# Kernel tuning notes

Measured on AMD Instinct MI355X. Metric: run time of the kernel, lower is better.

## Reference

```python
import math
import jax, jax.numpy as jnp
import numpy as np

B, L, H = 32, 1024, 128

def setup_inputs() -> dict:
    key = jax.random.key(0)
    k1, k2, k3, k4 = jax.random.split(key, 4)
    a = jax.random.normal(k1, (B, L, H), dtype=jnp.float32)
    b = jax.random.normal(k2, (B, L, H), dtype=jnp.float32)
    mask_a = jax.random.randint(k3, (B, L, 1), 0, 2, dtype=jnp.int32)
    mask_b = jax.random.randint(k4, (B, L, 1), 0, 2, dtype=jnp.int32)
    temperature = jnp.asarray(1.0 / math.sqrt(H), dtype=jnp.float32)
    return {"a": a, "b": b, "mask_a": mask_a, "mask_b": mask_b, "temperature": temperature}

def reference(a, b, mask_a, mask_b, temperature):
    # scores: [B, La, Lb]
    scores = jnp.einsum('bld,bmd->blm', a, b) * temperature
    # outer product of token validity masks -> pair mask [B, La, Lb]
    mask = jnp.einsum('blk,bmk->blm', mask_a.astype(jnp.float32), mask_b.astype(jnp.float32)) > 0
    scores = jnp.where(mask, scores, jnp.float32(-10000.0))
    attention_a = jax.nn.softmax(scores, axis=1)  # normalize over La (columns)
    attention_b = jax.nn.softmax(scores, axis=2)  # normalize over Lb (rows)
    feature_a = jnp.einsum('blm,bmd->bld', attention_b, b)
    feature_b = jnp.einsum('blm,bmd->bld', attention_a, a)  # valid since La == Lb
    return (feature_a, feature_b)
```

## Files before the change

kernel.cpp:

```cpp
#include <hip/hip_runtime.h>
#include <math.h>

#define BN 32
#define LL 1024
#define HH 128

typedef __attribute__((ext_vector_type(8))) short short8;
typedef __attribute__((ext_vector_type(4))) float f32x4;

static const size_t SZ_BF = (size_t)BN * LL * HH * 2;

__device__ __forceinline__ ushort f2bf(float x) {
  union { float f; unsigned u; } c; c.f = x;
  unsigned r = c.u + 0x7fffu + ((c.u >> 16) & 1u);
  return (ushort)(r >> 16);
}
__device__ __forceinline__ float bf2f(ushort h) {
  union { unsigned u; float f; } c; c.u = ((unsigned)h) << 16;
  return c.f;
}
__device__ __forceinline__ short8 ld8(const ushort* p) {
  return *(const short8*)p;
}

__global__ __launch_bounds__(256) void k_convert(
    const float* __restrict__ a, const float* __restrict__ b,
    const int* __restrict__ mask_b,
    ushort* __restrict__ abf, ushort* __restrict__ bbf,
    ushort* __restrict__ aT, ushort* __restrict__ bT,
    float* __restrict__ meanb, float* __restrict__ invmean) {
  int bb = blockIdx.y;
  int l0 = blockIdx.x * 64;
  int which = blockIdx.z;
  const float* src = which ? b : a;
  ushort* dst  = which ? bbf : abf;
  ushort* dstT = which ? bT : aT;
  float* dmean = which ? meanb : invmean;
  __shared__ __align__(16) ushort T[128][72];
  __shared__ float accS[128];
  __shared__ float wgt[64];
  int t = threadIdx.x;
  if (t < 128) accS[t] = 0.f;
  if (t < 64)
    wgt[t] = which ? 1.0f : ((mask_b[bb * LL + l0 + t] == 0) ? 1.0f : 0.0f);
  int lrow = t >> 5;
  int dcol = (t & 31) * 4;
#pragma unroll
  for (int p = 0; p < 8; ++p) {
    int l = p * 8 + lrow;
    float4 v = *(const float4*)&src[((size_t)bb * LL + l0 + l) * HH + dcol];
    ushort4 u;
    u.x = f2bf(v.x); u.y = f2bf(v.y); u.z = f2bf(v.z); u.w = f2bf(v.w);
    *(ushort4*)&dst[((size_t)bb * LL + l0 + l) * HH + dcol] = u;
    T[dcol + 0][l] = u.x; T[dcol + 1][l] = u.y;
    T[dcol + 2][l] = u.z; T[dcol + 3][l] = u.w;
  }
  __syncthreads();
  int drow = t >> 3;
  int c8 = (t & 7) * 8;
#pragma unroll
  for (int q = 0; q < 4; ++q) {
    int d = q * 32 + drow;
    short8 val = *(const short8*)&T[d][c8];
    *(short8*)&dstT[((size_t)bb * HH + d) * LL + l0 + c8] = val;
    float s = 0.f;
#pragma unroll
    for (int j = 0; j < 8; ++j) s += wgt[c8 + j] * bf2f((ushort)val[j]);
    atomicAdd(&accS[d], s);
  }
  __syncthreads();
  if (t < 128) atomicAdd(&dmean[bb * HH + t], accS[t]);
}


__global__ __launch_bounds__(256, 2) void k_colsum(
    const ushort* __restrict__ abf, const ushort* __restrict__ bbf,
    const int* __restrict__ mask_a, const int* __restrict__ mask_b,
    const float* __restrict__ temp_p, float2* __restrict__ cc) {
  int wg = blockIdx.x;
  int xcd = wg & 7, k_ = wg >> 3;
  int bb = (k_ >> 4) * 8 + xcd;
  int m0 = (k_ & 15) * 64;
  int t = threadIdx.x;
  int w = t >> 6, lane = t & 63, l16 = lane & 15, quad = lane >> 4;
  float temp = temp_p[0];
  __shared__ __align__(16) float biasA[LL];
  __shared__ float csred[4][4][16];
  for (int i = t; i < LL; i += 256)
    biasA[i] = mask_a[bb * LL + i] ? 0.0f : -10000.0f;

  short8 Bm[4][4];
  float biasB_mt[4];
#pragma unroll
  for (int mt = 0; mt < 4; ++mt) {
    int m = m0 + mt * 16 + l16;
    biasB_mt[mt] = mask_b[bb * LL + m] ? 0.0f : -10000.0f;
#pragma unroll
    for (int k = 0; k < 4; ++k)
      Bm[mt][k] = ld8(&bbf[((size_t)bb * LL + m) * HH + k * 32 + quad * 8]);
  }
  __syncthreads();

  float cs[4] = {0.f, 0.f, 0.f, 0.f};
  short8 Al0[4], Al1[4];

#define LOADAL(AlX, IT)                                                       \
  {                                                                           \
    const ushort* arow = &abf[((size_t)bb * LL + w * 256 + (IT) * 16 + l16) * HH]; \
    _Pragma("unroll") for (int k = 0; k < 4; ++k)                             \
        AlX[k] = ld8(&arow[k * 32 + quad * 8]);                               \
  }

#define CSCOMPUTE(AlX, IT)                                                    \
  {                                                                           \
    int lbase = w * 256 + (IT) * 16;                                          \
    f32x4 bA = *(const f32x4*)&biasA[lbase + quad * 4];                       \
    _Pragma("unroll") for (int mt = 0; mt < 4; ++mt) {                        \
      f32x4 sacc = {0.f, 0.f, 0.f, 0.f};                                      \
      _Pragma("unroll") for (int k = 0; k < 4; ++k)                           \
          sacc = __builtin_amdgcn_mfma_f32_16x16x32_bf16(AlX[k], Bm[mt][k],   \
                                                         sacc, 0, 0, 0);      \
      _Pragma("unroll") for (int r = 0; r < 4; ++r)                           \
          cs[mt] += __expf(sacc[r] * temp + bA[r] + biasB_mt[mt]);            \
    }                                                                         \
  }

  LOADAL(Al0, 0);
  for (int it = 0; it < 16; it += 2) {
    LOADAL(Al1, it + 1);
    CSCOMPUTE(Al0, it);
    LOADAL(Al0, (it + 2) & 15);
    CSCOMPUTE(Al1, it + 1);
  }
#undef LOADAL
#undef CSCOMPUTE

#pragma unroll
  for (int mt = 0; mt < 4; ++mt) {
    cs[mt] += __shfl_xor(cs[mt], 16);
    cs[mt] += __shfl_xor(cs[mt], 32);
  }
  if (lane < 16) {
#pragma unroll
    for (int mt = 0; mt < 4; ++mt) csred[w][mt][l16] = cs[mt];
  }
  __syncthreads();
  if (t < 64) {
    int mt = t >> 4, ml = t & 15;
    float s = csred[0][mt][ml] + csred[1][mt][ml] + csred[2][mt][ml] + csred[3][mt][ml];
    int m = m0 + t;
    float bB = mask_b[bb * LL + m] ? 0.0f : -10000.0f;
    cc[bb * LL + m] = make_float2(s > 0.f ? 1.0f / s : 0.0f, bB);
  }
}

__global__ __launch_bounds__(256, 2) void k_features(
    const ushort* __restrict__ abf, const ushort* __restrict__ bbf,
    const ushort* __restrict__ aT, const ushort* __restrict__ bT,
    const int* __restrict__ mask_a, const float* __restrict__ temp_p,
    const float2* __restrict__ cc, const float* __restrict__ meanb,
    const float* __restrict__ invmean, float* __restrict__ out) {
  int wg = blockIdx.x;
  int xcd = wg & 7, k_ = wg >> 3;
  int bb = (k_ >> 4) * 8 + xcd;
  int l0 = (k_ & 15) * 64;
  int t = threadIdx.x;
  int w = t >> 6, lane = t & 63, l16 = lane & 15, quad = lane >> 4;
  float temp = temp_p[0];

  __shared__ float2 ccs[LL];
  __shared__ __align__(16) ushort Pa[2][64 * 72];
  __shared__ __align__(16) ushort Pb[2][64 * 72];
  __shared__ float rspart[4][64];
  __shared__ float rsfin[64];

  for (int i = t; i < LL; i += 256) ccs[i] = cc[bb * LL + i];

  float biasA_lt[4];
  short8 Afix[4][4];
#pragma unroll
  for (int lt = 0; lt < 4; ++lt) {
    int l = l0 + lt * 16 + l16;
    biasA_lt[lt] = mask_a[bb * LL + l] ? 0.0f : -10000.0f;
#pragma unroll
    for (int k = 0; k < 4; ++k)
      Afix[lt][k] = ld8(&abf[((size_t)bb * LL + l) * HH + k * 32 + quad * 8]);
  }

  f32x4 accA[4][2], accB[4][2];
  f32x4 zero = {0.f, 0.f, 0.f, 0.f};
#pragma unroll
  for (int lt = 0; lt < 4; ++lt)
#pragma unroll
    for (int dt = 0; dt < 2; ++dt) { accA[lt][dt] = zero; accB[lt][dt] = zero; }
  float rs_lt[4] = {0.f, 0.f, 0.f, 0.f};
  __syncthreads();

  short8 Am0[4], Am1[4];
  float2 cv0[4], cv1[4];
  short8 Bb0[2][2], Ba0[2][2], Bb1[2][2], Ba1[2][2];

#define LOADAM(AmX, cvX, M0)                                                  \
  {                                                                           \
    const ushort* brow = &bbf[((size_t)bb * LL + (M0) + w * 16 + l16) * HH];  \
    _Pragma("unroll") for (int k = 0; k < 4; ++k)                             \
        AmX[k] = ld8(&brow[k * 32 + quad * 8]);                               \
    _Pragma("unroll") for (int r = 0; r < 4; ++r)                             \
        cvX[r] = ccs[(M0) + w * 16 + quad * 4 + r];                           \
  }

#define LOADBT(BbX, BaX, M0)                                                  \
  {                                                                           \
    _Pragma("unroll") for (int dt = 0; dt < 2; ++dt) {                        \
      const ushort* btrow =                                                   \
          &bT[((size_t)bb * HH + w * 32 + dt * 16 + l16) * LL + (M0)];        \
      const ushort* atrow =                                                   \
          &aT[((size_t)bb * HH + w * 32 + dt * 16 + l16) * LL + (M0)];        \
      _Pragma("unroll") for (int ks = 0; ks < 2; ++ks) {                      \
        BbX[dt][ks] = ld8(&btrow[ks * 32 + quad * 8]);                        \
        BaX[dt][ks] = ld8(&atrow[ks * 32 + quad * 8]);                        \
      }                                                                       \
    }                                                                         \
  }

#define SPHASE(AmX, cvX, PBUFI)                                               \
  {                                                                           \
    ushort* pa = &Pa[PBUFI][0];                                               \
    ushort* pb = &Pb[PBUFI][0];                                               \
    _Pragma("unroll") for (int lt = 0; lt < 4; ++lt) {                        \
      f32x4 sacc = zero;                                                      \
      _Pragma("unroll") for (int k = 0; k < 4; ++k)                           \
          sacc = __builtin_amdgcn_mfma_f32_16x16x32_bf16(AmX[k], Afix[lt][k], \
                                                         sacc, 0, 0, 0);      \
      ushort pav[4], pbv[4];                                                  \
      _Pragma("unroll") for (int r = 0; r < 4; ++r) {                         \
        float e = __expf(sacc[r] * temp + biasA_lt[lt] + cvX[r].y);           \
        pav[r] = f2bf(e);                                                     \
        rs_lt[lt] += bf2f(pav[r]);                                            \
        pbv[r] = f2bf(e * cvX[r].x);                                          \
      }                                                                       \
      uint2 ka, kb;                                                           \
      ka.x = (uint)pav[0] | ((uint)pav[1] << 16);                             \
      ka.y = (uint)pav[2] | ((uint)pav[3] << 16);                             \
      kb.x = (uint)pbv[0] | ((uint)pbv[1] << 16);                             \
      kb.y = (uint)pbv[2] | ((uint)pbv[3] << 16);                             \
      int pidx = (lt * 16 + l16) * 72 + w * 16 + quad * 4;                    \
      *(uint2*)&pa[pidx] = ka;                                                \
      *(uint2*)&pb[pidx] = kb;                                                \
    }                                                                         \
  }

#define FPHASE(PBUFI, BbX, BaX)                                               \
  {                                                                           \
    const ushort* pa = &Pa[PBUFI][0];                                         \
    const ushort* pb = &Pb[PBUFI][0];                                         \
    _Pragma("unroll") for (int lt = 0; lt < 4; ++lt) {                        \
      _Pragma("unroll") for (int ks = 0; ks < 2; ++ks) {                      \
        int ridx = (lt * 16 + l16) * 72 + ks * 32 + quad * 8;                 \
        short8 PaF = *(const short8*)&pa[ridx];                               \
        short8 PbF = *(const short8*)&pb[ridx];                               \
        _Pragma("unroll") for (int dt = 0; dt < 2; ++dt) {                    \
          accA[lt][dt] = __builtin_amdgcn_mfma_f32_16x16x32_bf16(             \
              PaF, BbX[dt][ks], accA[lt][dt], 0, 0, 0);                       \
          accB[lt][dt] = __builtin_amdgcn_mfma_f32_16x16x32_bf16(             \
              PbF, BaX[dt][ks], accB[lt][dt], 0, 0, 0);                       \
        }                                                                     \
      }                                                                       \
    }                                                                         \
  }

  LOADAM(Am0, cv0, 0);
  LOADBT(Bb0, Ba0, 0);
  LOADAM(Am1, cv1, 64);
  SPHASE(Am0, cv0, 0);
  __syncthreads();

  for (int kk = 0; kk < 7; ++kk) {
    int mA = (2 * kk + 1) * 64;
    LOADBT(Bb1, Ba1, mA);
    LOADAM(Am0, cv0, mA + 64);
    SPHASE(Am1, cv1, 1);
    FPHASE(0, Bb0, Ba0);
    __syncthreads();
    LOADBT(Bb0, Ba0, mA + 64);
    LOADAM(Am1, cv1, mA + 128);
    SPHASE(Am0, cv0, 0);
    FPHASE(1, Bb1, Ba1);
    __syncthreads();
  }

  LOADBT(Bb1, Ba1, 960);
  SPHASE(Am1, cv1, 1);
  FPHASE(0, Bb0, Ba0);
  __syncthreads();
  FPHASE(1, Bb1, Ba1);

#undef LOADAM
#undef LOADBT
#undef SPHASE
#undef FPHASE

#pragma unroll
  for (int lt = 0; lt < 4; ++lt) {
    rs_lt[lt] += __shfl_xor(rs_lt[lt], 16);
    rs_lt[lt] += __shfl_xor(rs_lt[lt], 32);
  }
  if (lane < 16) {
#pragma unroll
    for (int lt = 0; lt < 4; ++lt) rspart[w][lt * 16 + l16] = rs_lt[lt];
  }
  __syncthreads();
  if (t < 64)
    rsfin[t] = rspart[0][t] + rspart[1][t] + rspart[2][t] + rspart[3][t];
  __syncthreads();

  float* outA = out;
  float* outB = out + (size_t)BN * LL * HH;
#pragma unroll
  for (int dt = 0; dt < 2; ++dt) {
    int d = w * 32 + dt * 16 + l16;
    float mb = meanb[bb * HH + d] * (1.0f / 1024.0f);
    float im = invmean[bb * HH + d] * (1.0f / 1024.0f);
#pragma unroll
    for (int lt = 0; lt < 4; ++lt) {
#pragma unroll
      for (int r = 0; r < 4; ++r) {
        int l = lt * 16 + quad * 4 + r;
        float rsv = rsfin[l];
        float fa = (rsv > 0.f) ? accA[lt][dt][r] / rsv : mb;
        float fb = accB[lt][dt][r] + im;
        __builtin_nontemporal_store(fa, &outA[((size_t)bb * LL + l0 + l) * HH + d]);
        __builtin_nontemporal_store(fb, &outB[((size_t)bb * LL + l0 + l) * HH + d]);
      }
    }
  }
}

extern "C" void kernel_launch(void* const* d_in, const int* in_sizes, int n_in,
                              void* d_out, int out_size, void* d_ws, size_t ws_size,
                              hipStream_t stream) {
  const float* a = (const float*)d_in[0];
  const float* b = (const float*)d_in[1];
  const int* mask_a = (const int*)d_in[2];
  const int* mask_b = (const int*)d_in[3];
  const float* temp = (const float*)d_in[4];
  float* out = (float*)d_out;

  char* wsb = (char*)d_ws;
  ushort* abf = (ushort*)(wsb + 0 * SZ_BF);
  ushort* bbf = (ushort*)(wsb + 1 * SZ_BF);
  ushort* aT  = (ushort*)(wsb + 2 * SZ_BF);
  ushort* bT  = (ushort*)(wsb + 3 * SZ_BF);
  float2* cc  = (float2*)(wsb + 4 * SZ_BF);
  float* meanb   = (float*)(wsb + 4 * SZ_BF + (size_t)BN * LL * sizeof(float2));
  float* invmean = meanb + BN * HH;

  hipMemsetAsync(meanb, 0, 2 * BN * HH * sizeof(float), stream);
  k_convert<<<dim3(16, 32, 2), 256, 0, stream>>>(a, b, mask_b, abf, bbf, aT, bT,
                                                 meanb, invmean);
  k_colsum<<<dim3(512), 256, 0, stream>>>(abf, bbf, mask_a, mask_b, temp, cc);
  k_features<<<dim3(512), 256, 0, stream>>>(abf, bbf, aT, bT, mask_a, temp,
                                            cc, meanb, invmean, out);
  (void)in_sizes; (void)n_in; (void)out_size; (void)ws_size;
}
```

Measured before the change: 200.7 us.

## Fold column-softmax normalization into transposed A instead of a second P tile

The column-sum kernel now scales the transposed bf16 copy of A in place by each column's inverse softmax sum. The feature kernel can then reuse the single unnormalized P tile for both MFMA products. This drops the second LDS P buffer, its bf16 conversions, and its LDS writes and reads in the inner loop. In exchange, the colsum kernel does an extra read-modify-write pass over aT, and rounding shifts because the scaling is applied to A rather than to P.

```diff
diff --git a/kernel.cpp b/kernel.cpp
--- a/kernel.cpp
+++ b/kernel.cpp
@@ -75,6 +75,7 @@
 
 __global__ __launch_bounds__(256, 2) void k_colsum(
     const ushort* __restrict__ abf, const ushort* __restrict__ bbf,
+    ushort* __restrict__ aTm,
     const int* __restrict__ mask_a, const int* __restrict__ mask_b,
     const float* __restrict__ temp_p, float2* __restrict__ cc) {
   int wg = blockIdx.x;
@@ -86,6 +87,7 @@
   float temp = temp_p[0];
   __shared__ __align__(16) float biasA[LL];
   __shared__ float csred[4][4][16];
+  __shared__ float invS[64];
   for (int i = t; i < LL; i += 256)
     biasA[i] = mask_a[bb * LL + i] ? 0.0f : -10000.0f;
 
@@ -150,7 +152,28 @@
     float s = csred[0][mt][ml] + csred[1][mt][ml] + csred[2][mt][ml] + csred[3][mt][ml];
     int m = m0 + t;
     float bB = mask_b[bb * LL + m] ? 0.0f : -10000.0f;
-    cc[bb * LL + m] = make_float2(s > 0.f ? 1.0f / s : 0.0f, bB);
+    float inv = s > 0.f ? 1.0f / s : 0.0f;
+    invS[t] = inv;
+    cc[bb * LL + m] = make_float2(inv, bB);
+  }
+  __syncthreads();
+
+  {
+    int d = t >> 1, mc = (t & 1) * 32;
+    ushort* ap = &aTm[((size_t)bb * HH + d) * LL + m0 + mc];
+    short8 v0 = ld8(ap), v1 = ld8(ap + 8), v2 = ld8(ap + 16), v3 = ld8(ap + 24);
+    ushort o[32];
+#pragma unroll
+    for (int j = 0; j < 8; ++j) {
+      o[j]      = f2bf(bf2f((ushort)v0[j]) * invS[mc + j]);
+      o[8 + j]  = f2bf(bf2f((ushort)v1[j]) * invS[mc + 8 + j]);
+      o[16 + j] = f2bf(bf2f((ushort)v2[j]) * invS[mc + 16 + j]);
+      o[24 + j] = f2bf(bf2f((ushort)v3[j]) * invS[mc + 24 + j]);
+    }
+    *(short8*)ap        = *(short8*)&o[0];
+    *(short8*)(ap + 8)  = *(short8*)&o[8];
+    *(short8*)(ap + 16) = *(short8*)&o[16];
+    *(short8*)(ap + 24) = *(short8*)&o[24];
   }
 }
 
@@ -170,7 +193,6 @@
 
   __shared__ float2 ccs[LL];
   __shared__ __align__(16) ushort Pa[2][64 * 72];
-  __shared__ __align__(16) ushort Pb[2][64 * 72];
   __shared__ float rspart[4][64];
   __shared__ float rsfin[64];
 
@@ -197,7 +219,7 @@
   __syncthreads();
 
   short8 Am0[4], Am1[4];
-  float2 cv0[4], cv1[4];
+  float cv0[4], cv1[4];
   short8 Bb0[2][2], Ba0[2][2], Bb1[2][2], Ba1[2][2];
 
 #define LOADAM(AmX, cvX, M0)                                                  \
@@ -206,7 +228,7 @@
     _Pragma("unroll") for (int k = 0; k < 4; ++k)                             \
         AmX[k] = ld8(&brow[k * 32 + quad * 8]);                               \
     _Pragma("unroll") for (int r = 0; r < 4; ++r)                             \
-        cvX[r] = ccs[(M0) + w * 16 + quad * 4 + r];                           \
+        cvX[r] = ccs[(M0) + w * 16 + quad * 4 + r].y;                         \
   }
 
 #define LOADBT(BbX, BaX, M0)                                                  \
@@ -226,44 +248,37 @@
 #define SPHASE(AmX, cvX, PBUFI)                                               \
   {                                                                           \
     ushort* pa = &Pa[PBUFI][0];                                               \
-    ushort* pb = &Pb[PBUFI][0];                                               \
     _Pragma("unroll") for (int lt = 0; lt < 4; ++lt) {                        \
       f32x4 sacc = zero;                                                      \
       _Pragma("unroll") for (int k = 0; k < 4; ++k)                           \
           sacc = __builtin_amdgcn_mfma_f32_16x16x32_bf16(AmX[k], Afix[lt][k], \
                                                          sacc, 0, 0, 0);      \
-      ushort pav[4], pbv[4];                                                  \
+      ushort pav[4];                                                          \
       _Pragma("unroll") for (int r = 0; r < 4; ++r) {                         \
-        float e = __expf(sacc[r] * temp + biasA_lt[lt] + cvX[r].y);           \
+        float e = __expf(sacc[r] * temp + biasA_lt[lt] + cvX[r]);             \
         pav[r] = f2bf(e);                                                     \
         rs_lt[lt] += bf2f(pav[r]);                                            \
-        pbv[r] = f2bf(e * cvX[r].x);                                          \
       }                                                                       \
-      uint2 ka, kb;                                                           \
+      uint2 ka;                                                               \
       ka.x = (uint)pav[0] | ((uint)pav[1] << 16);                             \
       ka.y = (uint)pav[2] | ((uint)pav[3] << 16);                             \
-      kb.x = (uint)pbv[0] | ((uint)pbv[1] << 16);                             \
-      kb.y = (uint)pbv[2] | ((uint)pbv[3] << 16);                             \
       int pidx = (lt * 16 + l16) * 72 + w * 16 + quad * 4;                    \
       *(uint2*)&pa[pidx] = ka;                                                \
-      *(uint2*)&pb[pidx] = kb;                                                \
     }                                                                         \
   }
 
 #define FPHASE(PBUFI, BbX, BaX)                                               \
   {                                                                           \
     const ushort* pa = &Pa[PBUFI][0];                                         \
-    const ushort* pb = &Pb[PBUFI][0];                                         \
     _Pragma("unroll") for (int lt = 0; lt < 4; ++lt) {                        \
       _Pragma("unroll") for (int ks = 0; ks < 2; ++ks) {                      \
         int ridx = (lt * 16 + l16) * 72 + ks * 32 + quad * 8;                 \
         short8 PaF = *(const short8*)&pa[ridx];                               \
-        short8 PbF = *(const short8*)&pb[ridx];                               \
         _Pragma("unroll") for (int dt = 0; dt < 2; ++dt) {                    \
           accA[lt][dt] = __builtin_amdgcn_mfma_f32_16x16x32_bf16(             \
               PaF, BbX[dt][ks], accA[lt][dt], 0, 0, 0);                       \
           accB[lt][dt] = __builtin_amdgcn_mfma_f32_16x16x32_bf16(             \
-              PbF, BaX[dt][ks], accB[lt][dt], 0, 0, 0);                       \
+              PaF, BaX[dt][ks], accB[lt][dt], 0, 0, 0);                       \
         }                                                                     \
       }                                                                       \
     }                                                                         \
@@ -358,7 +373,7 @@
   hipMemsetAsync(meanb, 0, 2 * BN * HH * sizeof(float), stream);
   k_convert<<<dim3(16, 32, 2), 256, 0, stream>>>(a, b, mask_b, abf, bbf, aT, bT,
                                                  meanb, invmean);
-  k_colsum<<<dim3(512), 256, 0, stream>>>(abf, bbf, mask_a, mask_b, temp, cc);
+  k_colsum<<<dim3(512), 256, 0, stream>>>(abf, bbf, aT, mask_a, mask_b, temp, cc);
   k_features<<<dim3(512), 256, 0, stream>>>(abf, bbf, aT, bT, mask_a, temp,
                                             cc, meanb, invmean, out);
   (void)in_sizes; (void)n_in; (void)out_size; (void)ws_size;
```

After: 203.8 us. No clear change (+1.5%).
